# Performance work log

Hardware: AMD Instinct MI355X
Metric: run time of the kernel (lower is better)

The kernel has to match this reference:

```python
import jax, jax.numpy as jnp
import numpy as np

B, N, C, R, E = 8, 4096, 128, 16, 65536


def setup_inputs() -> dict:
    key = jax.random.key(0)
    ks = jax.random.split(key, 8)
    node_features = jax.random.normal(ks[0], (B, N, C), dtype=jnp.float32)
    edge_index = jax.random.randint(ks[1], (B, 2, E), 0, N, dtype=jnp.int64)
    edge_type = jax.random.randint(ks[2], (B, E), 0, R, dtype=jnp.int64)
    s = 1.0 / np.sqrt(C)
    rel_weight = jax.random.uniform(ks[3], (R, C, C), jnp.float32, -s, s)
    root_weight = jax.random.uniform(ks[4], (C, C), jnp.float32, -s, s)
    rgcn_bias = jnp.zeros((C,), jnp.float32)
    lin_weight = jax.random.uniform(ks[5], (C, 1), jnp.float32, -s, s)
    lin_bias = jnp.zeros((1,), jnp.float32)
    return {
        'node_features': node_features,
        'edge_index': edge_index,
        'edge_type': edge_type,
        'rel_weight': rel_weight,
        'root_weight': root_weight,
        'rgcn_bias': rgcn_bias,
        'lin_weight': lin_weight,
        'lin_bias': lin_bias,
    }


def _rgcn_score(node_features, edge_index, edge_type, rel_weight, root_weight,
                rgcn_bias, lin_weight, lin_bias):
    # Flatten batch of graphs into one big disjoint graph (as batch_rgcn does).
    x = node_features.reshape(B * N, C)
    offs = (jnp.arange(B, dtype=edge_index.dtype) * N)[:, None, None]  # (B,1,1)
    ei = (edge_index + offs).transpose(1, 0, 2).reshape(2, B * E)  # (2, B*E)
    et = edge_type.reshape(B * E)
    src, dst = ei[0], ei[1]

    x_src = x[src]  # (B*E, C) gathered source features
    # root transform + bias (RGCNConv root_weight + bias)
    out = x @ root_weight + rgcn_bias  # (B*N, C)
    # per-relation mean aggregation; mean(W_r x_j) == W_r mean(x_j)
    for r in range(R):
        mask = (et == r).astype(x.dtype)  # (B*E,)
        s = jax.ops.segment_sum(x_src * mask[:, None], dst, num_segments=B * N)
        cnt = jax.ops.segment_sum(mask, dst, num_segments=B * N)
        mean = jnp.where(cnt[:, None] > 0, s / jnp.maximum(cnt, 1.0)[:, None], 0.0)
        out = out + mean @ rel_weight[r]

    out = jax.nn.relu(out)  # dropout is identity at eval
    scores = (out @ lin_weight + lin_bias).reshape(B, N)
    return scores


def reference(node_features, edge_index, edge_type, rel_weight, root_weight,
              rgcn_bias, lin_weight, lin_bias):
    return _rgcn_score(node_features, edge_index, edge_type, rel_weight,
                       root_weight, rgcn_bias, lin_weight, lin_bias)
```

## Files before the change

kernel.cpp:

```cpp
#include <hip/hip_runtime.h>

#define BB 8
#define NN 4096
#define CC 128
#define RR 16
#define EE 65536
#define NNODES 32768
#define NEDGES 524288
#define BCAP  48
#define SCE   15
#define NT    32
#define ALP   136

typedef unsigned short ushort_t;
typedef short bf16x8 __attribute__((ext_vector_type(8)));
typedef float f32x4 __attribute__((ext_vector_type(4)));
typedef float f32x2 __attribute__((ext_vector_type(2)));

__device__ __forceinline__ unsigned short f2b(float f) {
    unsigned u = __builtin_bit_cast(unsigned, f);
    unsigned r = (u + 0x7fffu + ((u >> 16) & 1u)) >> 16;
    return (unsigned short)r;
}
__device__ __forceinline__ float b2f(unsigned short s) {
    return __builtin_bit_cast(float, (unsigned)s << 16);
}
__device__ __forceinline__ float ldf(const void* p, int j, int isbf) {
    return isbf ? b2f(((const ushort_t*)p)[j]) : ((const float*)p)[j];
}
__device__ __forceinline__ int ldi(const int* p, int j, int is64) {
    return p[j << is64];
}
__device__ __forceinline__ unsigned cvtpk(float lo, float hi) {
    unsigned r;
    asm("v_cvt_pk_bf16_f32 %0, %1, %2" : "=v"(r) : "v"(lo), "v"(hi));
    return r;
}
__device__ __forceinline__ float bcf(unsigned u) { return __builtin_bit_cast(float, u); }

#define GSUM8P(u) do { \
    s2[0] += (f32x2){bcf((u).x << 16), bcf((u).x & 0xffff0000u)}; \
    s2[1] += (f32x2){bcf((u).y << 16), bcf((u).y & 0xffff0000u)}; \
    s2[2] += (f32x2){bcf((u).z << 16), bcf((u).z & 0xffff0000u)}; \
    s2[3] += (f32x2){bcf((u).w << 16), bcf((u).w & 0xffff0000u)}; \
} while (0)
#define GSUM8P2(u) do { \
    s2[4] += (f32x2){bcf((u).x << 16), bcf((u).x & 0xffff0000u)}; \
    s2[5] += (f32x2){bcf((u).y << 16), bcf((u).y & 0xffff0000u)}; \
    s2[6] += (f32x2){bcf((u).z << 16), bcf((u).z & 0xffff0000u)}; \
    s2[7] += (f32x2){bcf((u).w << 16), bcf((u).w & 0xffff0000u)}; \
} while (0)

__global__ __launch_bounds__(256) void prep_k(const void* __restrict__ x,
                                              const void* __restrict__ relw,
                                              const void* __restrict__ rootw,
                                              const int* __restrict__ ei,
                                              const int* __restrict__ et,
                                              ushort_t* __restrict__ Xb,
                                              ushort_t* __restrict__ WT3,
                                              int* __restrict__ dcnt,
                                              int* __restrict__ bucket,
                                              int isbf, int w64i, int w64t) {
    int bx = blockIdx.x, t = threadIdx.x;
    if (bx < 1024) {
        int b = bx & 7;
        #pragma unroll
        for (int i = 0; i < 2; ++i) {
            int e = (bx >> 3) * 512 + i * 256 + t;
            int src = ldi(ei, (b * 2) * EE + e, w64i);
            int dst = ldi(ei, (b * 2 + 1) * EE + e, w64i);
            int r = ldi(et, (b << 16) + e, w64t);
            int gd = (b << 12) + dst;
            int pos = atomicAdd(&dcnt[gd << 4], 1);
            if (pos < BCAP)
                bucket[gd * BCAP + pos] = (((b << 12) + src) << 4) | r;
        }
    } else if (bx < 1536) {
        int bx2 = bx - 1024;
        int base = (bx2 & 7) * 65536 + (bx2 >> 3) * 256 + t;
        #pragma unroll
        for (int i = 0; i < 4; ++i) {
            int tid = base + i * 16384;
            if (isbf) {
                ((uint4*)Xb)[tid] = ((const uint4*)x)[tid];
            } else {
                const float4* xf = (const float4*)x;
                float4 a = xf[2 * tid], b = xf[2 * tid + 1];
                ushort4 o0, o1;
                o0.x = f2b(a.x); o0.y = f2b(a.y); o0.z = f2b(a.z); o0.w = f2b(a.w);
                o1.x = f2b(b.x); o1.y = f2b(b.y); o1.z = f2b(b.z); o1.w = f2b(b.w);
                ((ushort4*)Xb)[2 * tid] = o0; ((ushort4*)Xb)[2 * tid + 1] = o1;
            }
        }
    } else {
        __shared__ ushort_t Ls[128 * 40];
        int mb = bx - 1536;
        int mat = mb >> 2, chunk = mb & 3;
        const void* src = (mat == 16) ? rootw : relw;
        int soff = (mat == 16) ? 0 : mat * 16384;
        int k0 = chunk * 32;
        #pragma unroll
        for (int i = 0; i < 16; ++i) {
            int idx = t + i * 256;
            int k = idx >> 7, c = idx & 127;
            Ls[c * 40 + k] = f2b(ldf(src, soff + (k0 + k) * 128 + c, isbf));
        }
        __syncthreads();
        #pragma unroll
        for (int i = 0; i < 2; ++i) {
            int idx = t + i * 256;
            int cg = idx >> 6, lane = idx & 63;
            int lrow = lane & 15, lq = lane >> 4;
            uint4 v = *(const uint4*)(&Ls[(cg * 16 + lrow) * 40 + lq * 8]);
            *(uint4*)(WT3 + ((size_t)((mat * 4 + chunk) * 8 + cg)) * 512 + lane * 8) = v;
        }
    }
}

__global__ __launch_bounds__(256, 5) void agg_k(const ushort_t* __restrict__ Xb,
                                                const ushort_t* __restrict__ WT3,
                                                const int* __restrict__ dcnt,
                                                const int* __restrict__ bucket,
                                                const void* __restrict__ bias,
                                                const void* __restrict__ linw,
                                                const void* __restrict__ linb,
                                                void* __restrict__ out,
                                                int isbf) {
    __shared__ int scnt[NT * 16];
    __shared__ ushort_t srt[NT * 16 * 16];
    __shared__ ushort_t A[NT * ALP];
    __shared__ float red[NT][5];
    int bx = blockIdx.x, t = threadIdx.x;
    int n0 = (bx & 7) * NN + (bx >> 3) * NT;

    scnt[t] = 0; scnt[256 + t] = 0;
    __syncthreads();

    int nsub = t >> 3, tsub = t & 7;
    int gn = n0 + nsub;
    int offA = tsub * 8, offB = 64 + tsub * 8;
    int nc = dcnt[gn << 4]; if (nc > BCAP) nc = BCAP;
    const int* bk = bucket + gn * BCAP;
    for (int j = tsub; j < nc; j += 8) {
        int v = bk[j];
        int row = (nsub << 4) + (v & 15);
        int pos = atomicAdd(&scnt[row], 1);
        if (pos < SCE)
            srt[(row << 4) + 1 + pos] = (ushort_t)((unsigned)v >> 4);
    }
    __syncthreads();
    srt[t << 4] = (ushort_t)scnt[t];
    srt[(t + 256) << 4] = (ushort_t)scnt[t + 256];
    __syncthreads();

    int wave = t >> 6, lane = t & 63, lrow = lane & 15, lq = lane >> 4;
    f32x4 acc[2][2] = {};

    {
        int row = nsub << 4;
        uint4 q0 = *(const uint4*)(&srt[row << 4]);
        int cf = q0.x & 0xffffu; int ce = cf > SCE ? SCE : cf;
        f32x2 s2[8] = {};
        for (int e = 0; e < ce; ++e) {
            int gs = srt[(row << 4) + 1 + e];
            const ushort_t* xr = Xb + (size_t)gs * 128;
            uint4 ua = *(const uint4*)(xr + offA), ub = *(const uint4*)(xr + offB);
            GSUM8P(ua); GSUM8P2(ub);
        }
        f32x2 w2 = {0.f, 0.f};
        if (cf > 0) { float w = 1.0f / (float)cf; w2 = (f32x2){w, w}; }
        #pragma unroll
        for (int j = 0; j < 8; ++j) s2[j] *= w2;
        uint4 va, vb;
        va.x = cvtpk(s2[0].x, s2[0].y); va.y = cvtpk(s2[1].x, s2[1].y);
        va.z = cvtpk(s2[2].x, s2[2].y); va.w = cvtpk(s2[3].x, s2[3].y);
        vb.x = cvtpk(s2[4].x, s2[4].y); vb.y = cvtpk(s2[5].x, s2[5].y);
        vb.z = cvtpk(s2[6].x, s2[6].y); vb.w = cvtpk(s2[7].x, s2[7].y);
        *(uint4*)(&A[nsub * ALP + offA]) = va;
        *(uint4*)(&A[nsub * ALP + offB]) = vb;
    }
    __syncthreads();

    for (int p = 0; p < 17; ++p) {
        int np = p + 1;
        uint4 r0a, r0b, r1a, r1b, r2a, r2b, r3a, r3b;
        int cf = 0, ce = 0, row = 0;
        if (np < 16) {
            row = (nsub << 4) + np;
            uint4 q0 = *(const uint4*)(&srt[row << 4]);
            cf = q0.x & 0xffffu; ce = cf > SCE ? SCE : cf;
            int e0 = q0.x >> 16, e1 = q0.y & 0xffffu, e2 = q0.y >> 16, e3 = q0.z & 0xffffu;
            if (ce > 0) { const ushort_t* xr = Xb + (size_t)e0 * 128; r0a = *(const uint4*)(xr + offA); r0b = *(const uint4*)(xr + offB); }
            if (ce > 1) { const ushort_t* xr = Xb + (size_t)e1 * 128; r1a = *(const uint4*)(xr + offA); r1b = *(const uint4*)(xr + offB); }
            if (ce > 2) { const ushort_t* xr = Xb + (size_t)e2 * 128; r2a = *(const uint4*)(xr + offA); r2b = *(const uint4*)(xr + offB); }
            if (ce > 3) { const ushort_t* xr = Xb + (size_t)e3 * 128; r3a = *(const uint4*)(xr + offA); r3b = *(const uint4*)(xr + offB); }
        } else if (np == 16) {
            const ushort_t* xr = Xb + (size_t)gn * 128;
            r0a = *(const uint4*)(xr + offA); r0b = *(const uint4*)(xr + offB);
        }
        const ushort_t* bw = WT3 + (size_t)p * 16384 + (wave * 2) * 512 + lane * 8;
        __builtin_amdgcn_s_setprio(1);
        #pragma unroll
        for (int ks = 0; ks < 4; ++ks) {
            int k0 = ks * 32 + lq * 8;
            bf16x8 a0 = *(const bf16x8*)(&A[lrow * ALP + k0]);
            bf16x8 a1 = *(const bf16x8*)(&A[(16 + lrow) * ALP + k0]);
            bf16x8 b0 = *(const bf16x8*)(bw + ks * 4096);
            bf16x8 b1 = *(const bf16x8*)(bw + ks * 4096 + 512);
            acc[0][0] = __builtin_amdgcn_mfma_f32_16x16x32_bf16(a0, b0, acc[0][0], 0, 0, 0);
            acc[0][1] = __builtin_amdgcn_mfma_f32_16x16x32_bf16(a0, b1, acc[0][1], 0, 0, 0);
            acc[1][0] = __builtin_amdgcn_mfma_f32_16x16x32_bf16(a1, b0, acc[1][0], 0, 0, 0);
            acc[1][1] = __builtin_amdgcn_mfma_f32_16x16x32_bf16(a1, b1, acc[1][1], 0, 0, 0);
        }
        __builtin_amdgcn_s_setprio(0);
        if (p == 16) break;
        __syncthreads();
        if (np < 16) {
            f32x2 s2[8] = {};
            if (ce > 0) { GSUM8P(r0a); GSUM8P2(r0b); }
            if (ce > 1) { GSUM8P(r1a); GSUM8P2(r1b); }
            if (ce > 2) { GSUM8P(r2a); GSUM8P2(r2b); }
            if (ce > 3) { GSUM8P(r3a); GSUM8P2(r3b); }
            if (ce > 4) {
                for (int e4 = 4; e4 < ce; ++e4) {
                    int gs = srt[(row << 4) + 1 + e4];
                    const ushort_t* xr = Xb + (size_t)gs * 128;
                    uint4 ta = *(const uint4*)(xr + offA), tb = *(const uint4*)(xr + offB);
                    GSUM8P(ta); GSUM8P2(tb);
                }
            }
            f32x2 w2 = {0.f, 0.f};
            if (cf > 0) { float w = 1.0f / (float)cf; w2 = (f32x2){w, w}; }
            #pragma unroll
            for (int j = 0; j < 8; ++j) s2[j] *= w2;
            uint4 va, vb;
            va.x = cvtpk(s2[0].x, s2[0].y); va.y = cvtpk(s2[1].x, s2[1].y);
            va.z = cvtpk(s2[2].x, s2[2].y); va.w = cvtpk(s2[3].x, s2[3].y);
            vb.x = cvtpk(s2[4].x, s2[4].y); vb.y = cvtpk(s2[5].x, s2[5].y);
            vb.z = cvtpk(s2[6].x, s2[6].y); vb.w = cvtpk(s2[7].x, s2[7].y);
            *(uint4*)(&A[nsub * ALP + offA]) = va;
            *(uint4*)(&A[nsub * ALP + offB]) = vb;
        } else {
            *(uint4*)(&A[nsub * ALP + offA]) = r0a;
            *(uint4*)(&A[nsub * ALP + offB]) = r0b;
        }
        __syncthreads();
    }

    int wn = wave << 5;
    int c0 = wn + lrow, c1 = wn + 16 + lrow;
    float bi0 = ldf(bias, c0, isbf), bi1 = ldf(bias, c1, isbf);
    float lw0 = ldf(linw, c0, isbf), lw1 = ldf(linw, c1, isbf);
    #pragma unroll
    for (int mi = 0; mi < 2; ++mi)
        #pragma unroll
        for (int rg = 0; rg < 4; ++rg) {
            float p = fmaxf(acc[mi][0][rg] + bi0, 0.f) * lw0
                    + fmaxf(acc[mi][1][rg] + bi1, 0.f) * lw1;
            p += __shfl_xor(p, 1, 64);
            p += __shfl_xor(p, 2, 64);
            p += __shfl_xor(p, 4, 64);
            p += __shfl_xor(p, 8, 64);
            if (lrow == 0) red[mi * 16 + lq * 4 + rg][wave] = p;
        }
    __syncthreads();
    if (t < NT) {
        float res = red[t][0] + red[t][1] + red[t][2] + red[t][3] + ldf(linb, 0, isbf);
        if (isbf) ((ushort_t*)out)[n0 + t] = f2b(res);
        else      ((float*)out)[n0 + t] = res;
    }
}

extern "C" void kernel_launch(void* const* d_in, const int* in_sizes, int n_in,
                              void* d_out, int out_size, void* d_ws, size_t ws_size,
                              hipStream_t stream) {
    const void* x     = d_in[0];
    const int*  ei    = (const int*)d_in[1];
    const int*  et    = (const int*)d_in[2];
    const void* relw  = d_in[3];
    const void* rootw = d_in[4];
    const void* bias  = d_in[5];
    const void* linw  = d_in[6];
    const void* linb  = d_in[7];

    int isbf = (in_sizes[0] == BB * NN * CC * 2);
    int w64i = (in_sizes[1] == BB * 2 * EE * 8);
    int w64t = (in_sizes[2] == BB * EE * 8);

    const size_t WS_NEED = 17334272;
    if (ws_size < WS_NEED) return;

    char* ws = (char*)d_ws;
    ushort_t* Xb     = (ushort_t*)(ws);
    ushort_t* WT3    = (ushort_t*)(ws + 8388608);
    int*      dcnt   = (int*)(ws + 8945664);
    int*      bucket = (int*)(ws + 11042816);

    hipMemsetAsync(dcnt, 0, 2097152, stream);
    prep_k<<<1604, 256, 0, stream>>>(x, relw, rootw, ei, et, Xb, WT3, dcnt, bucket,
                                     isbf, w64i, w64t);
    agg_k<<<1024, 256, 0, stream>>>(Xb, WT3, dcnt, bucket, bias, linw, linb, d_out, isbf);
}
```

Before: 151.8 us.

## Double-buffer LDS A tile in agg_k and coarsen edge bucketing blocks

Gives agg_k two LDS buffers for the aggregated-feature tile, so the next relation's gather and sum is written into the other buffer while MFMAs read the current one. This removes one __syncthreads per relation step. Per-relation counts are now read straight from scnt, which drops the extra pass that stored counts into srt and raises the per-relation capacity from 15 to 16. In prep_k each bucketing block now handles 4 edge iterations instead of 2, halving those blocks. The cost is more LDS per block, with launch bounds lowered from 5 to 4 blocks per CU.

Result: faster. 146.1 us (-3.8%).

```diff
diff --git a/kernel.cpp b/kernel.cpp
--- a/kernel.cpp
+++ b/kernel.cpp
@@ -8,7 +8,7 @@
 #define NNODES 32768
 #define NEDGES 524288
 #define BCAP  48
-#define SCE   15
+#define SCAP  16
 #define NT    32
 #define ALP   136
 
@@ -38,13 +38,13 @@
 }
 __device__ __forceinline__ float bcf(unsigned u) { return __builtin_bit_cast(float, u); }
 
-#define GSUM8P(u) do { \
+#define GSUM8PA(u) do { \
     s2[0] += (f32x2){bcf((u).x << 16), bcf((u).x & 0xffff0000u)}; \
     s2[1] += (f32x2){bcf((u).y << 16), bcf((u).y & 0xffff0000u)}; \
     s2[2] += (f32x2){bcf((u).z << 16), bcf((u).z & 0xffff0000u)}; \
     s2[3] += (f32x2){bcf((u).w << 16), bcf((u).w & 0xffff0000u)}; \
 } while (0)
-#define GSUM8P2(u) do { \
+#define GSUM8PB(u) do { \
     s2[4] += (f32x2){bcf((u).x << 16), bcf((u).x & 0xffff0000u)}; \
     s2[5] += (f32x2){bcf((u).y << 16), bcf((u).y & 0xffff0000u)}; \
     s2[6] += (f32x2){bcf((u).z << 16), bcf((u).z & 0xffff0000u)}; \
@@ -62,11 +62,11 @@
                                               int* __restrict__ bucket,
                                               int isbf, int w64i, int w64t) {
     int bx = blockIdx.x, t = threadIdx.x;
-    if (bx < 1024) {
+    if (bx < 512) {
         int b = bx & 7;
         #pragma unroll
-        for (int i = 0; i < 2; ++i) {
-            int e = (bx >> 3) * 512 + i * 256 + t;
+        for (int i = 0; i < 4; ++i) {
+            int e = (bx >> 3) * 1024 + i * 256 + t;
             int src = ldi(ei, (b * 2) * EE + e, w64i);
             int dst = ldi(ei, (b * 2 + 1) * EE + e, w64i);
             int r = ldi(et, (b << 16) + e, w64t);
@@ -75,8 +75,8 @@
             if (pos < BCAP)
                 bucket[gd * BCAP + pos] = (((b << 12) + src) << 4) | r;
         }
-    } else if (bx < 1536) {
-        int bx2 = bx - 1024;
+    } else if (bx < 1024) {
+        int bx2 = bx - 512;
         int base = (bx2 & 7) * 65536 + (bx2 >> 3) * 256 + t;
         #pragma unroll
         for (int i = 0; i < 4; ++i) {
@@ -94,7 +94,7 @@
         }
     } else {
         __shared__ ushort_t Ls[128 * 40];
-        int mb = bx - 1536;
+        int mb = bx - 1024;
         int mat = mb >> 2, chunk = mb & 3;
         const void* src = (mat == 16) ? rootw : relw;
         int soff = (mat == 16) ? 0 : mat * 16384;
@@ -117,7 +117,7 @@
     }
 }
 
-__global__ __launch_bounds__(256, 5) void agg_k(const ushort_t* __restrict__ Xb,
+__global__ __launch_bounds__(256, 4) void agg_k(const ushort_t* __restrict__ Xb,
                                                 const ushort_t* __restrict__ WT3,
                                                 const int* __restrict__ dcnt,
                                                 const int* __restrict__ bucket,
@@ -127,8 +127,8 @@
                                                 void* __restrict__ out,
                                                 int isbf) {
     __shared__ int scnt[NT * 16];
-    __shared__ ushort_t srt[NT * 16 * 16];
-    __shared__ ushort_t A[NT * ALP];
+    __shared__ ushort_t srt[NT * 16 * SCAP];
+    __shared__ ushort_t A[2][NT * ALP];
     __shared__ float red[NT][5];
     int bx = blockIdx.x, t = threadIdx.x;
     int n0 = (bx & 7) * NN + (bx >> 3) * NT;
@@ -143,29 +143,24 @@
     const int* bk = bucket + gn * BCAP;
     for (int j = tsub; j < nc; j += 8) {
         int v = bk[j];
-        int row = (nsub << 4) + (v & 15);
-        int pos = atomicAdd(&scnt[row], 1);
-        if (pos < SCE)
-            srt[(row << 4) + 1 + pos] = (ushort_t)((unsigned)v >> 4);
-    }
-    __syncthreads();
-    srt[t << 4] = (ushort_t)scnt[t];
-    srt[(t + 256) << 4] = (ushort_t)scnt[t + 256];
+        int pos = atomicAdd(&scnt[(nsub << 4) + (v & 15)], 1);
+        if (pos < SCAP)
+            srt[(((nsub << 4) + (v & 15)) << 4) + pos] = (ushort_t)((unsigned)v >> 4);
+    }
     __syncthreads();
 
     int wave = t >> 6, lane = t & 63, lrow = lane & 15, lq = lane >> 4;
     f32x4 acc[2][2] = {};
 
     {
-        int row = nsub << 4;
-        uint4 q0 = *(const uint4*)(&srt[row << 4]);
-        int cf = q0.x & 0xffffu; int ce = cf > SCE ? SCE : cf;
+        int cf = scnt[nsub << 4];
+        int ce = cf > SCAP ? SCAP : cf;
+        const ushort_t* lst = &srt[nsub << 8];
         f32x2 s2[8] = {};
         for (int e = 0; e < ce; ++e) {
-            int gs = srt[(row << 4) + 1 + e];
-            const ushort_t* xr = Xb + (size_t)gs * 128;
+            const ushort_t* xr = Xb + (size_t)lst[e] * 128;
             uint4 ua = *(const uint4*)(xr + offA), ub = *(const uint4*)(xr + offB);
-            GSUM8P(ua); GSUM8P2(ub);
+            GSUM8PA(ua); GSUM8PB(ub);
         }
         f32x2 w2 = {0.f, 0.f};
         if (cf > 0) { float w = 1.0f / (float)cf; w2 = (f32x2){w, w}; }
@@ -176,35 +171,37 @@
         va.z = cvtpk(s2[2].x, s2[2].y); va.w = cvtpk(s2[3].x, s2[3].y);
         vb.x = cvtpk(s2[4].x, s2[4].y); vb.y = cvtpk(s2[5].x, s2[5].y);
         vb.z = cvtpk(s2[6].x, s2[6].y); vb.w = cvtpk(s2[7].x, s2[7].y);
-        *(uint4*)(&A[nsub * ALP + offA]) = va;
-        *(uint4*)(&A[nsub * ALP + offB]) = vb;
+        *(uint4*)(&A[0][nsub * ALP + offA]) = va;
+        *(uint4*)(&A[0][nsub * ALP + offB]) = vb;
     }
     __syncthreads();
 
     for (int p = 0; p < 17; ++p) {
         int np = p + 1;
         uint4 r0a, r0b, r1a, r1b, r2a, r2b, r3a, r3b;
-        int cf = 0, ce = 0, row = 0;
+        int cf = 0, ce = 0;
         if (np < 16) {
-            row = (nsub << 4) + np;
-            uint4 q0 = *(const uint4*)(&srt[row << 4]);
-            cf = q0.x & 0xffffu; ce = cf > SCE ? SCE : cf;
-            int e0 = q0.x >> 16, e1 = q0.y & 0xffffu, e2 = q0.y >> 16, e3 = q0.z & 0xffffu;
-            if (ce > 0) { const ushort_t* xr = Xb + (size_t)e0 * 128; r0a = *(const uint4*)(xr + offA); r0b = *(const uint4*)(xr + offB); }
-            if (ce > 1) { const ushort_t* xr = Xb + (size_t)e1 * 128; r1a = *(const uint4*)(xr + offA); r1b = *(const uint4*)(xr + offB); }
-            if (ce > 2) { const ushort_t* xr = Xb + (size_t)e2 * 128; r2a = *(const uint4*)(xr + offA); r2b = *(const uint4*)(xr + offB); }
-            if (ce > 3) { const ushort_t* xr = Xb + (size_t)e3 * 128; r3a = *(const uint4*)(xr + offA); r3b = *(const uint4*)(xr + offB); }
+            cf = scnt[(nsub << 4) + np];
+            ce = cf > SCAP ? SCAP : cf;
+            uint4 q0 = *(const uint4*)(&srt[((nsub << 4) + np) << 4]);
+            int e0 = q0.x & 0xffffu, e1 = q0.x >> 16;
+            int e2i = q0.y & 0xffffu, e3 = q0.y >> 16;
+            if (ce > 0) { const ushort_t* xr = Xb + (size_t)e0 * 128;  r0a = *(const uint4*)(xr + offA); r0b = *(const uint4*)(xr + offB); }
+            if (ce > 1) { const ushort_t* xr = Xb + (size_t)e1 * 128;  r1a = *(const uint4*)(xr + offA); r1b = *(const uint4*)(xr + offB); }
+            if (ce > 2) { const ushort_t* xr = Xb + (size_t)e2i * 128; r2a = *(const uint4*)(xr + offA); r2b = *(const uint4*)(xr + offB); }
+            if (ce > 3) { const ushort_t* xr = Xb + (size_t)e3 * 128;  r3a = *(const uint4*)(xr + offA); r3b = *(const uint4*)(xr + offB); }
         } else if (np == 16) {
             const ushort_t* xr = Xb + (size_t)gn * 128;
             r0a = *(const uint4*)(xr + offA); r0b = *(const uint4*)(xr + offB);
         }
+        const ushort_t* Ap = A[p & 1];
         const ushort_t* bw = WT3 + (size_t)p * 16384 + (wave * 2) * 512 + lane * 8;
         __builtin_amdgcn_s_setprio(1);
         #pragma unroll
         for (int ks = 0; ks < 4; ++ks) {
             int k0 = ks * 32 + lq * 8;
-            bf16x8 a0 = *(const bf16x8*)(&A[lrow * ALP + k0]);
-            bf16x8 a1 = *(const bf16x8*)(&A[(16 + lrow) * ALP + k0]);
+            bf16x8 a0 = *(const bf16x8*)(&Ap[lrow * ALP + k0]);
+            bf16x8 a1 = *(const bf16x8*)(&Ap[(16 + lrow) * ALP + k0]);
             bf16x8 b0 = *(const bf16x8*)(bw + ks * 4096);
             bf16x8 b1 = *(const bf16x8*)(bw + ks * 4096 + 512);
             acc[0][0] = __builtin_amdgcn_mfma_f32_16x16x32_bf16(a0, b0, acc[0][0], 0, 0, 0);
@@ -213,20 +210,18 @@
             acc[1][1] = __builtin_amdgcn_mfma_f32_16x16x32_bf16(a1, b1, acc[1][1], 0, 0, 0);
         }
         __builtin_amdgcn_s_setprio(0);
-        if (p == 16) break;
-        __syncthreads();
         if (np < 16) {
             f32x2 s2[8] = {};
-            if (ce > 0) { GSUM8P(r0a); GSUM8P2(r0b); }
-            if (ce > 1) { GSUM8P(r1a); GSUM8P2(r1b); }
-            if (ce > 2) { GSUM8P(r2a); GSUM8P2(r2b); }
-            if (ce > 3) { GSUM8P(r3a); GSUM8P2(r3b); }
+            if (ce > 0) { GSUM8PA(r0a); GSUM8PB(r0b); }
+            if (ce > 1) { GSUM8PA(r1a); GSUM8PB(r1b); }
+            if (ce > 2) { GSUM8PA(r2a); GSUM8PB(r2b); }
+            if (ce > 3) { GSUM8PA(r3a); GSUM8PB(r3b); }
             if (ce > 4) {
+                const ushort_t* lst = &srt[((nsub << 4) + np) << 4];
                 for (int e4 = 4; e4 < ce; ++e4) {
-                    int gs = srt[(row << 4) + 1 + e4];
-                    const ushort_t* xr = Xb + (size_t)gs * 128;
+                    const ushort_t* xr = Xb + (size_t)lst[e4] * 128;
                     uint4 ta = *(const uint4*)(xr + offA), tb = *(const uint4*)(xr + offB);
-                    GSUM8P(ta); GSUM8P2(tb);
+                    GSUM8PA(ta); GSUM8PB(tb);
                 }
             }
             f32x2 w2 = {0.f, 0.f};
@@ -238,13 +233,13 @@
             va.z = cvtpk(s2[2].x, s2[2].y); va.w = cvtpk(s2[3].x, s2[3].y);
             vb.x = cvtpk(s2[4].x, s2[4].y); vb.y = cvtpk(s2[5].x, s2[5].y);
             vb.z = cvtpk(s2[6].x, s2[6].y); vb.w = cvtpk(s2[7].x, s2[7].y);
-            *(uint4*)(&A[nsub * ALP + offA]) = va;
-            *(uint4*)(&A[nsub * ALP + offB]) = vb;
-        } else {
-            *(uint4*)(&A[nsub * ALP + offA]) = r0a;
-            *(uint4*)(&A[nsub * ALP + offB]) = r0b;
-        }
-        __syncthreads();
+            *(uint4*)(&A[np & 1][nsub * ALP + offA]) = va;
+            *(uint4*)(&A[np & 1][nsub * ALP + offB]) = vb;
+        } else if (np == 16) {
+            *(uint4*)(&A[np & 1][nsub * ALP + offA]) = r0a;
+            *(uint4*)(&A[np & 1][nsub * ALP + offB]) = r0b;
+        }
+        if (p < 16) __syncthreads();
     }
 
     int wn = wave << 5;
@@ -297,7 +292,7 @@
     int*      bucket = (int*)(ws + 11042816);
 
     hipMemsetAsync(dcnt, 0, 2097152, stream);
-    prep_k<<<1604, 256, 0, stream>>>(x, relw, rootw, ei, et, Xb, WT3, dcnt, bucket,
+    prep_k<<<1092, 256, 0, stream>>>(x, relw, rootw, ei, et, Xb, WT3, dcnt, bucket,
                                      isbf, w64i, w64t);
     agg_k<<<1024, 256, 0, stream>>>(Xb, WT3, dcnt, bucket, bias, linw, linb, d_out, isbf);
 }
```
